# Kernel tuning notes

Measured on AMD Instinct MI355X. Metric: run time of the kernel, lower is better.

The kernel has to match this reference:

```python
import jax, jax.numpy as jnp
import numpy as np
import math

N, E, G = 10000, 100000, 500
HID, H = 128, 4
C = HID                      # out_channels per head (PyG TransformerConv)
NFREQ, NSPACE = 10, 3
EDIM = 2 * NFREQ * NSPACE    # 60 = dis_emb.dim
LAT, DIS = 6, 3
IN_DIM = HID + LAT + DIS     # 137
EPS = 1e-5


def _lin_init(k, fan_in, shape):
    b = 1.0 / math.sqrt(fan_in)
    return jax.random.uniform(k, shape, jnp.float32, -b, b)


def setup_inputs() -> dict:
    key = jax.random.key(0)
    ks = jax.random.split(key, 12)
    return dict(
        node_features=jax.random.normal(ks[0], (N, HID), jnp.float32),
        frac_coords=jax.random.uniform(ks[1], (N, DIS), jnp.float32),
        lattice_feats=jax.random.normal(ks[2], (G, LAT), jnp.float32),
        edge_index=jax.random.randint(ks[3], (2, E), 0, N),
        node2graph=jnp.sort(jax.random.randint(ks[4], (N,), 0, G)),
        frac_diff=jax.random.normal(ks[5], (E, DIS), jnp.float32) * 0.1,
        ln_gamma=jnp.ones((HID,), jnp.float32),
        ln_beta=jnp.zeros((HID,), jnp.float32),
        Wq=_lin_init(ks[6], IN_DIM, (IN_DIM, H * C)), bq=jnp.zeros((H * C,), jnp.float32),
        Wk=_lin_init(ks[7], IN_DIM, (IN_DIM, H * C)), bk=jnp.zeros((H * C,), jnp.float32),
        Wv=_lin_init(ks[8], IN_DIM, (IN_DIM, H * C)), bv=jnp.zeros((H * C,), jnp.float32),
        We=_lin_init(ks[9], EDIM, (EDIM, H * C)),
        Wskip=_lin_init(ks[10], IN_DIM, (IN_DIM, C)), bskip=jnp.zeros((C,), jnp.float32),
    )


def _sinusoids(frac_diff):
    # SinusoidsEmbedding: emb = x[...,None]*2*pi*arange(F); cat(sin, cos); detached
    freqs = 2.0 * jnp.pi * jnp.arange(NFREQ, dtype=jnp.float32)    # [F]
    emb = frac_diff[:, :, None] * freqs[None, None, :]             # [E,3,F]
    emb = emb.reshape(-1, NSPACE * NFREQ)                          # [E,30]
    return jnp.concatenate([jnp.sin(emb), jnp.cos(emb)], axis=-1)  # [E,60]


def _segment_softmax(scores, idx, num_segments):
    # softmax over variable-size neighborhoods grouped by target node idx
    m = jax.ops.segment_max(scores, idx, num_segments=num_segments)
    ex = jnp.exp(scores - m[idx])
    s = jax.ops.segment_sum(ex, idx, num_segments=num_segments)
    return ex / (s[idx] + 1e-16)


def reference(node_features, frac_coords, lattice_feats, edge_index, node2graph,
              frac_diff, ln_gamma, ln_beta, Wq, bq, Wk, bk, Wv, bv, We, Wskip, bskip):
    edge_emb = jax.lax.stop_gradient(_sinusoids(frac_diff))  # .detach() in original
    node_input = node_features
    # LayerNorm (biased variance, torch default)
    mu = node_features.mean(-1, keepdims=True)
    var = node_features.var(-1, keepdims=True)
    h = (node_features - mu) * jax.lax.rsqrt(var + EPS) * ln_gamma + ln_beta
    # gather per-graph lattice features to nodes, concat
    lat = lattice_feats.reshape(-1, LAT)[node2graph]                # [N,6]
    x = jnp.concatenate([h, lat, frac_coords], axis=1)              # [N,137]

    q = (x @ Wq + bq).reshape(N, H, C)
    k = (x @ Wk + bk).reshape(N, H, C)
    v = (x @ Wv + bv).reshape(N, H, C)
    e = (edge_emb @ We).reshape(E, H, C)                            # lin_edge (no bias)

    src, dst = edge_index[0], edge_index[1]  # message flows src -> dst (PyG default)
    k_e = k[src] + e                                                # [E,H,C]
    alpha = (q[dst] * k_e).sum(-1) / math.sqrt(C)                   # [E,H]
    alpha = _segment_softmax(alpha, dst, N)
    msg = (v[src] + e) * alpha[:, :, None]                          # [E,H,C]
    out = jax.ops.segment_sum(msg, dst, num_segments=N)             # [N,H,C]
    out = out.mean(axis=1)                                          # concat=False -> head mean
    out = out + (x @ Wskip + bskip)                                 # root skip connection
    return node_input + jax.nn.silu(out)
```

## Files before the change

### kernel.cpp

```cpp
#include <hip/hip_runtime.h>
#include <math.h>

#define N_NODES 10000
#define N_EDGES 100000
#define HIDDEN  128
#define NHEAD   4
#define CHAN    128
#define IN_DIM  137
#define KPAD    160
#define NCOLS   1904
#define NPAD    1920
#define LATD    6
#define DISD    3

#define PREP_BLOCKS 2500
#define TRANS_TILES 26
#define WQE_BLOCKS  150
#define WEBT_BLOCKS 128

#define SCAT_BLOCKS ((N_EDGES + 255) / 256)
#define GEMM_BX 15
#define GEMM_BY ((N_NODES + 63) / 64)
#define NR16    628
#define FRAG_STRIDE (5 * 64 * 8)

typedef __attribute__((ext_vector_type(8))) short short8v;
typedef __attribute__((ext_vector_type(4))) float float4v;
typedef __attribute__((ext_vector_type(2))) float float2v;

__device__ inline unsigned short f2bf(float f) {
    unsigned u = __float_as_uint(f);
    unsigned r = 0x7fffu + ((u >> 16) & 1u);
    return (unsigned short)((u + r) >> 16);
}
__device__ inline float bf2f(unsigned short u) {
    return __uint_as_float(((unsigned)u) << 16);
}
__device__ inline size_t frag_off(int grp16, int ks, int lane) {
    return (((size_t)grp16 * 5 + ks) * 64 + lane) * 8;
}
__device__ inline size_t frag_elem(int grp16, int lr, int k) {
    const int ks = k >> 5, g = (k >> 3) & 3, e = k & 7;
    return frag_off(grp16, ks, g * 16 + lr) + e;
}

__global__ __launch_bounds__(256) void prep_weights_kernel(
    const float* __restrict__ nf, const float* __restrict__ frac,
    const float* __restrict__ lat, const int* __restrict__ n2g,
    const float* __restrict__ gamma, const float* __restrict__ beta,
    const float* __restrict__ Wq, const float* __restrict__ bq,
    const float* __restrict__ Wk, const float* __restrict__ bk,
    const float* __restrict__ Wv, const float* __restrict__ bv,
    const float* __restrict__ Wsk, const float* __restrict__ bsk,
    const float* __restrict__ We,
    unsigned short* __restrict__ xfrag, int* __restrict__ hist,
    unsigned short* __restrict__ wfrag, float* __restrict__ bias_all,
    unsigned short* __restrict__ webt)
{
    __shared__ __align__(16) unsigned short Tlds[64 * 168];
    const int tid = threadIdx.x;

    if (blockIdx.x < PREP_BLOCKS) {
        int wave = tid >> 6;
        int lane = tid & 63;
        int n = blockIdx.x * 4 + wave;
        if (n >= N_NODES) return;

        float v0 = nf[n * HIDDEN + lane];
        float v1 = nf[n * HIDDEN + 64 + lane];
        float s  = v0 + v1;
        float sq = v0 * v0 + v1 * v1;
        #pragma unroll
        for (int m = 1; m < 64; m <<= 1) {
            s  += __shfl_xor(s, m);
            sq += __shfl_xor(sq, m);
        }
        float mean = s * (1.0f / 128.0f);
        float var  = sq * (1.0f / 128.0f) - mean * mean;
        float inv  = rsqrtf(var + 1e-5f);

        const int r16 = n >> 4, lr = n & 15;
        xfrag[frag_elem(r16, lr, lane)] =
            f2bf((v0 - mean) * inv * gamma[lane] + beta[lane]);
        xfrag[frag_elem(r16, lr, 64 + lane)] =
            f2bf((v1 - mean) * inv * gamma[64 + lane] + beta[64 + lane]);
        if (lane < LATD)
            xfrag[frag_elem(r16, lr, HIDDEN + lane)] = f2bf(lat[n2g[n] * LATD + lane]);
        if (lane < DISD)
            xfrag[frag_elem(r16, lr, HIDDEN + LATD + lane)] = f2bf(frac[n * DISD + lane]);
        if (lane >= 41)
            xfrag[frag_elem(r16, lr, 96 + lane)] = 0;
        if (lane == 0) hist[n] = 0;
    } else if (blockIdx.x < PREP_BLOCKS + TRANS_TILES) {
        const int n0 = (blockIdx.x - PREP_BLOCKS) * 64;
        for (int i = tid; i < 160 * 64; i += 256) {
            const int k = i >> 6, n = i & 63;
            const int col = n0 + n;
            float val = 0.0f;
            if (k < IN_DIM) {
                if (col < 512)        val = Wq[(size_t)k * 512 + col];
                else if (col < 1024)  val = Wk[(size_t)k * 512 + (col - 512)];
                else if (col < 1536)  val = Wv[(size_t)k * 512 + (col - 1024)];
                else                  val = Wsk[(size_t)k * 128 + (col - 1536)];
            }
            Tlds[n * 168 + k] = f2bf(val);
        }
        __syncthreads();
        for (int i = tid; i < 4 * 5 * 64; i += 256) {
            const int lane = i & 63;
            const int ks   = (i >> 6) % 5;
            const int c16l = i / (5 * 64);
            const int lr = lane & 15, g = lane >> 4;
            const int lcol = c16l * 16 + lr;
            const int k0 = ks * 32 + g * 8;
            const short8v v = *reinterpret_cast<const short8v*>(&Tlds[lcol * 168 + k0]);
            *reinterpret_cast<short8v*>(
                &wfrag[frag_off((n0 >> 4) + c16l, ks, lane)]) = v;
        }
        if (tid < 64) {
            const int col = n0 + tid;
            float b;
            if (col < 512)        b = bq[col];
            else if (col < 1024)  b = bk[col - 512];
            else if (col < 1536)  b = bv[col - 1024];
            else                  b = bsk[col - 1536];
            bias_all[col] = b;
        }
    } else if (blockIdx.x < PREP_BLOCKS + TRANS_TILES + WQE_BLOCKS) {
        int idx = (blockIdx.x - PREP_BLOCKS - TRANS_TILES) * 256 + tid;
        if (idx >= 240 * KPAD) return;
        int hj = idx / KPAD, k = idx % KPAD;
        int h = hj / 60, j = hj % 60;
        float s = 0.0f;
        if (k < IN_DIM) {
            #pragma unroll 4
            for (int c = 0; c < 128; ++c)
                s += Wq[(size_t)k * 512 + h * 128 + c] * We[(size_t)j * 512 + h * 128 + c];
        }
        const int col = 1664 + hj;
        wfrag[frag_elem(col >> 4, col & 15, k)] = f2bf(s);
        if (k == KPAD - 1) {
            float b = 0.0f;
            #pragma unroll 4
            for (int c = 0; c < 128; ++c)
                b += bq[h * 128 + c] * We[(size_t)j * 512 + h * 128 + c];
            bias_all[col] = b;
        }
    } else {
        int g = (blockIdx.x - PREP_BLOCKS - TRANS_TILES - WQE_BLOCKS) * 256 + tid;
        if (g >= 4 * 128 * 64) return;
        int h = g >> 13, c = (g >> 6) & 127, j = g & 63;
        float v = (j < 60) ? We[(size_t)j * 512 + h * 128 + c] : 0.0f;
        webt[g] = f2bf(v);
    }
}

__global__ __launch_bounds__(256) void hist_kernel(
    const int* __restrict__ eidx, int* __restrict__ hist)
{
    int e = blockIdx.x * 256 + threadIdx.x;
    if (e < N_EDGES) atomicAdd(&hist[eidx[N_EDGES + e]], 1);
}

__global__ __launch_bounds__(1024) void scan_kernel(
    const int* __restrict__ hist, int* __restrict__ offsets, int* __restrict__ cursor)
{
    __shared__ int part[1024];
    const int t = threadIdx.x;
    const int base = t * 10;
    int loc[10];
    int s = 0;
    #pragma unroll
    for (int i = 0; i < 10; ++i) {
        int v = (base + i < N_NODES) ? hist[base + i] : 0;
        loc[i] = s; s += v;
    }
    part[t] = s;
    __syncthreads();
    for (int off = 1; off < 1024; off <<= 1) {
        int v = (t >= off) ? part[t - off] : 0;
        __syncthreads();
        part[t] += v;
        __syncthreads();
    }
    int pre = (t > 0) ? part[t - 1] : 0;
    #pragma unroll
    for (int i = 0; i < 10; ++i)
        if (base + i < N_NODES) {
            offsets[base + i] = pre + loc[i];
            cursor[base + i]  = pre + loc[i];
        }
    if (t == 1023) offsets[N_NODES] = part[1023];
}

__global__ __launch_bounds__(256, 4) void gemm_scatter_kernel(
    const unsigned short* __restrict__ xfrag, const unsigned short* __restrict__ wfrag,
    const float* __restrict__ bias_all,
    const int* __restrict__ eidx, const float* __restrict__ fdiff,
    int* __restrict__ cursor, int* __restrict__ sorted_src,
    float* __restrict__ sorted_fd,
    float* __restrict__ sq, unsigned short* __restrict__ qbuf,
    unsigned char* __restrict__ kvb)
{
    if (blockIdx.x < SCAT_BLOCKS) {
        int e = blockIdx.x * 256 + threadIdx.x;
        if (e >= N_EDGES) return;
        int src = eidx[e];
        int dst = eidx[N_EDGES + e];
        int pos = atomicAdd(&cursor[dst], 1);
        sorted_src[pos] = src;
        sorted_fd[pos * 3 + 0] = fdiff[e * 3 + 0];
        sorted_fd[pos * 3 + 1] = fdiff[e * 3 + 1];
        sorted_fd[pos * 3 + 2] = fdiff[e * 3 + 2];
        return;
    }

    const int bx   = blockIdx.x - SCAT_BLOCKS;
    const int row0 = (bx / GEMM_BX) * 64;
    const int col0 = (bx % GEMM_BX) * 128;
    const int tid  = threadIdx.x;
    const int l    = tid & 63;
    const int wid  = tid >> 6;
    const int wr   = (wid >> 1) * 32;
    const int wc   = (wid & 1) * 64;
    const int lr   = l & 15;
    const int r16  = (row0 + wr) >> 4;
    const int c16  = (col0 + wc) >> 4;

    short8v a[2][5];
    #pragma unroll
    for (int ks = 0; ks < 5; ++ks)
        #pragma unroll
        for (int t = 0; t < 2; ++t)
            a[t][ks] = *reinterpret_cast<const short8v*>(
                &xfrag[frag_off(r16 + t, ks, l)]);

    float4v acc[2][4];
    #pragma unroll
    for (int tr = 0; tr < 2; ++tr)
        #pragma unroll
        for (int tc = 0; tc < 4; ++tc)
            acc[tr][tc] = (float4v){0.0f, 0.0f, 0.0f, 0.0f};

    #pragma unroll
    for (int ks = 0; ks < 5; ++ks) {
        short8v b[4];
        #pragma unroll
        for (int t = 0; t < 4; ++t)
            b[t] = *reinterpret_cast<const short8v*>(
                &wfrag[frag_off(c16 + t, ks, l)]);
        #pragma unroll
        for (int tr = 0; tr < 2; ++tr)
            #pragma unroll
            for (int tc = 0; tc < 4; ++tc)
                acc[tr][tc] = __builtin_amdgcn_mfma_f32_16x16x32_bf16(
                    a[tr][ks], b[tc], acc[tr][tc], 0, 0, 0);
    }

    #pragma unroll
    for (int tr = 0; tr < 2; ++tr) {
        #pragma unroll
        for (int tc = 0; tc < 4; ++tc) {
            const int col  = col0 + wc + tc * 16 + lr;
            const float bias = bias_all[col];
            #pragma unroll
            for (int j = 0; j < 4; ++j) {
                const int row = row0 + wr + tr * 16 + (l >> 4) * 4 + j;
                if (row < N_NODES) {
                    float val = acc[tr][tc][j] + bias;
                    if (col < 512) {
                        qbuf[(size_t)row * 512 + col] = f2bf(val);
                    } else if (col < 1024) {
                        const int h = (col - 512) >> 7, ck = (col - 512) & 127;
                        int p = __builtin_amdgcn_cvt_pk_fp8_f32(val, val, 0, false);
                        kvb[((size_t)row * 4 + h) * 256 + ck] = (unsigned char)(p & 0xFF);
                    } else if (col < 1536) {
                        const int h = (col - 1024) >> 7, cv = (col - 1024) & 127;
                        int p = __builtin_amdgcn_cvt_pk_fp8_f32(val, val, 0, false);
                        kvb[((size_t)row * 4 + h) * 256 + 128 + cv] = (unsigned char)(p & 0xFF);
                    } else if (col < 1664) {
                        sq[(size_t)row * 384 + (col - 1536)] = val;
                    } else if (col < NCOLS) {
                        sq[(size_t)row * 384 + 128 + (col - 1664)] = val;
                    }
                }
            }
        }
    }
}

__global__ __launch_bounds__(256) void gather_kernel(
    const float* __restrict__ sq, const unsigned short* __restrict__ qbuf,
    const unsigned char* __restrict__ kvb,
    const int* __restrict__ offsets, const int* __restrict__ sorted_src,
    const float* __restrict__ sorted_fd,
    unsigned short* __restrict__ avbh, unsigned short* __restrict__ aggbuf,
    float* __restrict__ sumwbuf)
{
    const int n    = blockIdx.x;
    const int h    = threadIdx.x >> 6;
    const int l    = threadIdx.x & 63;
    const int hl   = l & 31;
    const int half = l >> 5;
    const float TWO_PI = 6.283185307179586f;
    const float scale  = 0.08838834764831845f;

    const ushort4 qv = *reinterpret_cast<const ushort4*>(
        &qbuf[(size_t)n * 512 + h * 128 + 4 * hl]);
    const float q4x = bf2f(qv.x), q4y = bf2f(qv.y);
    const float q4z = bf2f(qv.z), q4w = bf2f(qv.w);
    const float qe_a = sq[(size_t)n * 384 + 128 + h * 60 + hl];
    const bool  v2ok = (hl < 28);
    const float qe_b = v2ok ? sq[(size_t)n * 384 + 128 + h * 60 + hl + 32] : 0.0f;

    const int   jj1  = (hl < 30) ? hl : hl - 30;
    const int   sd1  = jj1 / 10;
    const float fc1  = TWO_PI * (float)(jj1 % 10);
    const bool  sin1 = (hl < 30);
    const int   jj2  = hl + 2;
    const int   sd2  = v2ok ? (jj2 / 10) : 0;
    const float fc2  = v2ok ? TWO_PI * (float)(jj2 % 10) : 0.0f;

    float ax = 0.f, ay = 0.f, az = 0.f, aw = 0.f;
    float agg1 = 0.f, agg2 = 0.f, sumw = 0.f;
    const int e0 = offsets[n], e1 = offsets[n + 1];

    for (int base = e0; base < e1; base += 4) {
        const int eA = base + half;
        const int eB = base + half + 2;
        const bool okA = (eA < e1), okB = (eB < e1);
        const int iA = okA ? eA : e0;
        const int iB = okB ? eB : e0;
        const int srcA = sorted_src[iA];
        const int srcB = sorted_src[iB];
        const float fdA1 = sorted_fd[iA * 3 + sd1];
        const float fdA2 = sorted_fd[iA * 3 + sd2];
        const float fdB1 = sorted_fd[iB * 3 + sd1];
        const float fdB2 = sorted_fd[iB * 3 + sd2];
        const unsigned char* pA = kvb + ((size_t)srcA * 4 + h) * 256;
        const unsigned char* pB = kvb + ((size_t)srcB * 4 + h) * 256;
        const unsigned kAu = *reinterpret_cast<const unsigned*>(pA + 4 * hl);
        const unsigned vAu = *reinterpret_cast<const unsigned*>(pA + 128 + 4 * hl);
        const unsigned kBu = *reinterpret_cast<const unsigned*>(pB + 4 * hl);
        const unsigned vBu = *reinterpret_cast<const unsigned*>(pB + 128 + 4 * hl);

        const float eA1 = sin1 ? __sinf(fdA1 * fc1) : __cosf(fdA1 * fc1);
        const float eA2 = __cosf(fdA2 * fc2);
        const float eB1 = sin1 ? __sinf(fdB1 * fc1) : __cosf(fdB1 * fc1);
        const float eB2 = __cosf(fdB2 * fc2);

        const float2v kA01 = __builtin_amdgcn_cvt_pk_f32_fp8(kAu, false);
        const float2v kA23 = __builtin_amdgcn_cvt_pk_f32_fp8(kAu, true);
        const float2v kB01 = __builtin_amdgcn_cvt_pk_f32_fp8(kBu, false);
        const float2v kB23 = __builtin_amdgcn_cvt_pk_f32_fp8(kBu, true);

        float pAs = q4x * kA01[0] + q4y * kA01[1]
                  + q4z * kA23[0] + q4w * kA23[1]
                  + eA1 * qe_a + eA2 * qe_b;
        float pBs = q4x * kB01[0] + q4y * kB01[1]
                  + q4z * kB23[0] + q4w * kB23[1]
                  + eB1 * qe_a + eB2 * qe_b;
        #pragma unroll
        for (int m = 1; m <= 16; m <<= 1) {
            pAs += __shfl_xor(pAs, m);
            pBs += __shfl_xor(pBs, m);
        }
        const float wA = okA ? __expf(pAs * scale) : 0.0f;
        const float wB = okB ? __expf(pBs * scale) : 0.0f;
        sumw += wA + wB;

        const float2v vA01 = __builtin_amdgcn_cvt_pk_f32_fp8(vAu, false);
        const float2v vA23 = __builtin_amdgcn_cvt_pk_f32_fp8(vAu, true);
        const float2v vB01 = __builtin_amdgcn_cvt_pk_f32_fp8(vBu, false);
        const float2v vB23 = __builtin_amdgcn_cvt_pk_f32_fp8(vBu, true);
        ax += wA * vA01[0] + wB * vB01[0];
        ay += wA * vA01[1] + wB * vB01[1];
        az += wA * vA23[0] + wB * vB23[0];
        aw += wA * vA23[1] + wB * vB23[1];
        agg1 += wA * eA1 + wB * eB1;
        if (v2ok) agg2 += wA * eA2 + wB * eB2;
    }

    sumw += __shfl_xor(sumw, 32);
    ax += __shfl_xor(ax, 32);  ay += __shfl_xor(ay, 32);
    az += __shfl_xor(az, 32);  aw += __shfl_xor(aw, 32);
    agg1 += __shfl_xor(agg1, 32);
    agg2 += __shfl_xor(agg2, 32);

    if (half == 0) {
        ushort4 r;
        r.x = f2bf(ax); r.y = f2bf(ay); r.z = f2bf(az); r.w = f2bf(aw);
        *reinterpret_cast<ushort4*>(&avbh[(size_t)n * 512 + h * 128 + 4 * hl]) = r;
        aggbuf[n * 256 + h * 64 + hl]      = f2bf(agg1);
        aggbuf[n * 256 + h * 64 + 32 + hl] = f2bf(agg2);
        if (hl == 0) sumwbuf[n * 4 + h] = sumw;
    }
}

__global__ __launch_bounds__(256) void corrfin_kernel(
    const unsigned short* __restrict__ webt, const unsigned short* __restrict__ aggbuf,
    const unsigned short* __restrict__ avbh, const float* __restrict__ sumwbuf,
    const float* __restrict__ sq, const float* __restrict__ nf,
    float* __restrict__ out)
{
    const int node0 = blockIdx.x * 64;
    const int tid = threadIdx.x;
    const int l   = tid & 63;
    const int w   = tid >> 6;
    const int lr  = l & 15;
    const int lk  = (l >> 4) * 8;
    const int nbase = node0 + w * 16;

    float4v acc[4][8];
    #pragma unroll
    for (int h = 0; h < 4; ++h)
        #pragma unroll
        for (int nn = 0; nn < 8; ++nn)
            acc[h][nn] = (float4v){0.0f, 0.0f, 0.0f, 0.0f};

    const int arow = (nbase + lr < N_NODES) ? (nbase + lr) : 0;
    #pragma unroll
    for (int h = 0; h < 4; ++h) {
        #pragma unroll
        for (int ks = 0; ks < 2; ++ks) {
            const short8v a = *reinterpret_cast<const short8v*>(
                &aggbuf[(size_t)arow * 256 + h * 64 + ks * 32 + lk]);
            #pragma unroll
            for (int nn = 0; nn < 8; ++nn) {
                const short8v b = *reinterpret_cast<const short8v*>(
                    &webt[(size_t)(h * 128 + nn * 16 + lr) * 64 + ks * 32 + lk]);
                acc[h][nn] = __builtin_amdgcn_mfma_f32_16x16x32_bf16(a, b, acc[h][nn], 0, 0, 0);
            }
        }
    }

    float inv_sw[4][4];
    #pragma unroll
    for (int j = 0; j < 4; ++j) {
        const int node = nbase + (l >> 4) * 4 + j;
        const int nrd  = (node < N_NODES) ? node : 0;
        #pragma unroll
        for (int h = 0; h < 4; ++h)
            inv_sw[j][h] = 1.0f / (sumwbuf[nrd * 4 + h] + 1e-16f);
    }

    #pragma unroll
    for (int nn = 0; nn < 8; ++nn) {
        const int col = nn * 16 + lr;
        #pragma unroll
        for (int j = 0; j < 4; ++j) {
            const int node = nbase + (l >> 4) * 4 + j;
            if (node < N_NODES) {
                float z = 0.0f;
                #pragma unroll
                for (int h = 0; h < 4; ++h)
                    z += (bf2f(avbh[(size_t)node * 512 + h * 128 + col]) + acc[h][nn][j])
                         * inv_sw[j][h];
                z = 0.25f * z + sq[(size_t)node * 384 + col];
                float si = z / (1.0f + __expf(-z));
                out[node * CHAN + col] = nf[node * CHAN + col] + si;
            }
        }
    }
}

extern "C" void kernel_launch(void* const* d_in, const int* in_sizes, int n_in,
                              void* d_out, int out_size, void* d_ws, size_t ws_size,
                              hipStream_t stream)
{
    const float* nf    = (const float*)d_in[0];
    const float* frac  = (const float*)d_in[1];
    const float* lat   = (const float*)d_in[2];
    const int*   eidx  = (const int*)  d_in[3];
    const int*   n2g   = (const int*)  d_in[4];
    const float* fdiff = (const float*)d_in[5];
    const float* gamma = (const float*)d_in[6];
    const float* beta  = (const float*)d_in[7];
    const float* Wq    = (const float*)d_in[8];
    const float* bq    = (const float*)d_in[9];
    const float* Wk    = (const float*)d_in[10];
    const float* bk    = (const float*)d_in[11];
    const float* Wv    = (const float*)d_in[12];
    const float* bv    = (const float*)d_in[13];
    const float* We    = (const float*)d_in[14];
    const float* Wsk   = (const float*)d_in[15];
    const float* bsk   = (const float*)d_in[16];
    float* out = (float*)d_out;

    float* sq        = (float*)d_ws;
    float* sumwbuf   = sq + (size_t)N_NODES * 384;
    float* bias_all  = sumwbuf + (size_t)N_NODES * 4;
    float* sorted_fd = bias_all + NPAD;
    unsigned short* xfrag  = (unsigned short*)(sorted_fd + (size_t)N_EDGES * 3);
    unsigned short* wfrag  = xfrag + (size_t)NR16 * FRAG_STRIDE;
    unsigned short* webt   = wfrag + (size_t)(NPAD / 16) * FRAG_STRIDE;
    unsigned short* aggbuf = webt + 4 * 128 * 64;
    unsigned short* qbuf   = aggbuf + (size_t)N_NODES * 256;
    unsigned short* avbh   = qbuf + (size_t)N_NODES * 512;
    unsigned char*  kvb    = (unsigned char*)(avbh + (size_t)N_NODES * 512);
    int* hist       = (int*)(kvb + (size_t)N_NODES * 4 * 256);
    int* offsets    = hist + N_NODES;
    int* cursor     = offsets + N_NODES + 1;
    int* sorted_src = cursor + N_NODES;

    prep_weights_kernel<<<PREP_BLOCKS + TRANS_TILES + WQE_BLOCKS + WEBT_BLOCKS,
                          256, 0, stream>>>(
        nf, frac, lat, n2g, gamma, beta,
        Wq, bq, Wk, bk, Wv, bv, Wsk, bsk, We,
        xfrag, hist, wfrag, bias_all, webt);

    hist_kernel<<<(N_EDGES + 255) / 256, 256, 0, stream>>>(eidx, hist);
    scan_kernel<<<1, 1024, 0, stream>>>(hist, offsets, cursor);

    gemm_scatter_kernel<<<SCAT_BLOCKS + GEMM_BX * GEMM_BY, 256, 0, stream>>>(
        xfrag, wfrag, bias_all, eidx, fdiff, cursor, sorted_src, sorted_fd,
        sq, qbuf, kvb);

    gather_kernel<<<N_NODES, 256, 0, stream>>>(
        sq, qbuf, kvb, offsets, sorted_src, sorted_fd, avbh, aggbuf, sumwbuf);

    corrfin_kernel<<<(N_NODES + 63) / 64, 256, 0, stream>>>(
        webt, aggbuf, avbh, sumwbuf, sq, nf, out);
}
```

Baseline: 130.0 us.

## Interleave fp8 K/V per lane and stage We in LDS for Wq·We fold

The K/V fp8 buffer is now laid out with each lane's 4 K bytes and 4 V bytes adjacent, so the edge gather loop issues one 8-byte load per source instead of two 4-byte loads from separate halves. Separately, the Wq·We precompute blocks now cache a head's We slice in shared memory and each block handles a 16-row k chunk, cutting redundant global reads of We and the block count. Shared memory per block grows to 30 KB, which may reduce occupancy of the large prep kernel.

After: 139.3 us. 1.07x slower.

```diff
diff --git a/kernel.cpp b/kernel.cpp
--- a/kernel.cpp
+++ b/kernel.cpp
@@ -15,7 +15,7 @@
 
 #define PREP_BLOCKS 2500
 #define TRANS_TILES 26
-#define WQE_BLOCKS  150
+#define WQE_BLOCKS  40
 #define WEBT_BLOCKS 128
 
 #define SCAT_BLOCKS ((N_EDGES + 255) / 256)
@@ -57,7 +57,9 @@
     unsigned short* __restrict__ wfrag, float* __restrict__ bias_all,
     unsigned short* __restrict__ webt)
 {
-    __shared__ __align__(16) unsigned short Tlds[64 * 168];
+    __shared__ __align__(16) unsigned char smem[60 * 128 * 4];
+    unsigned short* Tlds = (unsigned short*)smem;
+    float*          WeL  = (float*)smem;
     const int tid = threadIdx.x;
 
     if (blockIdx.x < PREP_BLOCKS) {
@@ -127,24 +129,34 @@
             bias_all[col] = b;
         }
     } else if (blockIdx.x < PREP_BLOCKS + TRANS_TILES + WQE_BLOCKS) {
-        int idx = (blockIdx.x - PREP_BLOCKS - TRANS_TILES) * 256 + tid;
-        if (idx >= 240 * KPAD) return;
-        int hj = idx / KPAD, k = idx % KPAD;
-        int h = hj / 60, j = hj % 60;
-        float s = 0.0f;
-        if (k < IN_DIM) {
-            #pragma unroll 4
-            for (int c = 0; c < 128; ++c)
-                s += Wq[(size_t)k * 512 + h * 128 + c] * We[(size_t)j * 512 + h * 128 + c];
-        }
-        const int col = 1664 + hj;
-        wfrag[frag_elem(col >> 4, col & 15, k)] = f2bf(s);
-        if (k == KPAD - 1) {
-            float b = 0.0f;
-            #pragma unroll 4
-            for (int c = 0; c < 128; ++c)
-                b += bq[h * 128 + c] * We[(size_t)j * 512 + h * 128 + c];
-            bias_all[col] = b;
+        const int wb = blockIdx.x - PREP_BLOCKS - TRANS_TILES;
+        const int h  = wb / 10;
+        const int kc = wb % 10;
+        for (int i = tid; i < 60 * 128; i += 256) {
+            const int j = i >> 7, c = i & 127;
+            WeL[i] = We[(size_t)j * 512 + h * 128 + c];
+        }
+        __syncthreads();
+        for (int t = tid; t < 960; t += 256) {
+            const int j  = t >> 4;
+            const int kk = t & 15;
+            const int k  = kc * 16 + kk;
+            float s = 0.0f;
+            if (k < IN_DIM) {
+                const float* wq = &Wq[(size_t)k * 512 + h * 128];
+                #pragma unroll 4
+                for (int c = 0; c < 128; ++c)
+                    s += wq[c] * WeL[j * 128 + c];
+            }
+            const int col = 1664 + h * 60 + j;
+            wfrag[frag_elem(col >> 4, col & 15, k)] = f2bf(s);
+            if (k == KPAD - 1) {
+                float b = 0.0f;
+                #pragma unroll 4
+                for (int c = 0; c < 128; ++c)
+                    b += bq[h * 128 + c] * WeL[j * 128 + c];
+                bias_all[col] = b;
+            }
         }
     } else {
         int g = (blockIdx.x - PREP_BLOCKS - TRANS_TILES - WQE_BLOCKS) * 256 + tid;
@@ -273,11 +285,13 @@
                     } else if (col < 1024) {
                         const int h = (col - 512) >> 7, ck = (col - 512) & 127;
                         int p = __builtin_amdgcn_cvt_pk_fp8_f32(val, val, 0, false);
-                        kvb[((size_t)row * 4 + h) * 256 + ck] = (unsigned char)(p & 0xFF);
+                        kvb[((size_t)row * 4 + h) * 256 + (ck >> 2) * 8 + (ck & 3)]
+                            = (unsigned char)(p & 0xFF);
                     } else if (col < 1536) {
                         const int h = (col - 1024) >> 7, cv = (col - 1024) & 127;
                         int p = __builtin_amdgcn_cvt_pk_fp8_f32(val, val, 0, false);
-                        kvb[((size_t)row * 4 + h) * 256 + 128 + cv] = (unsigned char)(p & 0xFF);
+                        kvb[((size_t)row * 4 + h) * 256 + (cv >> 2) * 8 + 4 + (cv & 3)]
+                            = (unsigned char)(p & 0xFF);
                     } else if (col < 1664) {
                         sq[(size_t)row * 384 + (col - 1536)] = val;
                     } else if (col < NCOLS) {
@@ -337,22 +351,20 @@
         const float fdA2 = sorted_fd[iA * 3 + sd2];
         const float fdB1 = sorted_fd[iB * 3 + sd1];
         const float fdB2 = sorted_fd[iB * 3 + sd2];
-        const unsigned char* pA = kvb + ((size_t)srcA * 4 + h) * 256;
-        const unsigned char* pB = kvb + ((size_t)srcB * 4 + h) * 256;
-        const unsigned kAu = *reinterpret_cast<const unsigned*>(pA + 4 * hl);
-        const unsigned vAu = *reinterpret_cast<const unsigned*>(pA + 128 + 4 * hl);
-        const unsigned kBu = *reinterpret_cast<const unsigned*>(pB + 4 * hl);
-        const unsigned vBu = *reinterpret_cast<const unsigned*>(pB + 128 + 4 * hl);
+        const uint2 kvA = *reinterpret_cast<const uint2*>(
+            kvb + ((size_t)srcA * 4 + h) * 256 + 8 * hl);
+        const uint2 kvB = *reinterpret_cast<const uint2*>(
+            kvb + ((size_t)srcB * 4 + h) * 256 + 8 * hl);
 
         const float eA1 = sin1 ? __sinf(fdA1 * fc1) : __cosf(fdA1 * fc1);
         const float eA2 = __cosf(fdA2 * fc2);
         const float eB1 = sin1 ? __sinf(fdB1 * fc1) : __cosf(fdB1 * fc1);
         const float eB2 = __cosf(fdB2 * fc2);
 
-        const float2v kA01 = __builtin_amdgcn_cvt_pk_f32_fp8(kAu, false);
-        const float2v kA23 = __builtin_amdgcn_cvt_pk_f32_fp8(kAu, true);
-        const float2v kB01 = __builtin_amdgcn_cvt_pk_f32_fp8(kBu, false);
-        const float2v kB23 = __builtin_amdgcn_cvt_pk_f32_fp8(kBu, true);
+        const float2v kA01 = __builtin_amdgcn_cvt_pk_f32_fp8(kvA.x, false);
+        const float2v kA23 = __builtin_amdgcn_cvt_pk_f32_fp8(kvA.x, true);
+        const float2v kB01 = __builtin_amdgcn_cvt_pk_f32_fp8(kvB.x, false);
+        const float2v kB23 = __builtin_amdgcn_cvt_pk_f32_fp8(kvB.x, true);
 
         float pAs = q4x * kA01[0] + q4y * kA01[1]
                   + q4z * kA23[0] + q4w * kA23[1]
@@ -369,10 +381,10 @@
         const float wB = okB ? __expf(pBs * scale) : 0.0f;
         sumw += wA + wB;
 
-        const float2v vA01 = __builtin_amdgcn_cvt_pk_f32_fp8(vAu, false);
-        const float2v vA23 = __builtin_amdgcn_cvt_pk_f32_fp8(vAu, true);
-        const float2v vB01 = __builtin_amdgcn_cvt_pk_f32_fp8(vBu, false);
-        const float2v vB23 = __builtin_amdgcn_cvt_pk_f32_fp8(vBu, true);
+        const float2v vA01 = __builtin_amdgcn_cvt_pk_f32_fp8(kvA.y, false);
+        const float2v vA23 = __builtin_amdgcn_cvt_pk_f32_fp8(kvA.y, true);
+        const float2v vB01 = __builtin_amdgcn_cvt_pk_f32_fp8(kvB.y, false);
+        const float2v vB23 = __builtin_amdgcn_cvt_pk_f32_fp8(kvB.y, true);
         ax += wA * vA01[0] + wB * vB01[0];
         ay += wA * vA01[1] + wB * vB01[1];
         az += wA * vA23[0] + wB * vB23[0];
```
